# Optimization experiments

Measured on AMD Instinct MI355X. Metric: run time of the kernel, lower is better.

The kernel has to match this reference:

```python
import jax, jax.numpy as jnp
import numpy as np

D_MODEL = 1024
NUM_HEADS = 16
HEAD_DIM = D_MODEL // NUM_HEADS


def setup_inputs() -> dict:
    key = jax.random.key(0)
    kx, kq, kk, kv, ko = jax.random.split(key, 5)
    B, S = 4, 2048
    scale = 1.0 / np.sqrt(D_MODEL)
    return {
        "x": jax.random.normal(kx, (B, S, D_MODEL), dtype=jnp.float32),
        # bias-free linear weights, torch convention [out, in]
        "wq": jax.random.normal(kq, (D_MODEL, D_MODEL), dtype=jnp.float32) * scale,
        "wk": jax.random.normal(kk, (D_MODEL, D_MODEL), dtype=jnp.float32) * scale,
        "wv": jax.random.normal(kv, (D_MODEL, D_MODEL), dtype=jnp.float32) * scale,
        "wo": jax.random.normal(ko, (D_MODEL, D_MODEL), dtype=jnp.float32) * scale,
    }


def reference(x, wq, wk, wv, wo):
    B, S, D = x.shape
    H, Hd = NUM_HEADS, HEAD_DIM
    # projections (y = x @ W^T), reshape to [B, H, S, Hd]
    def proj(w):
        return jnp.einsum('bsd,ed->bse', x, w).reshape(B, S, H, Hd).transpose(0, 2, 1, 3)
    q, k, v = proj(wq), proj(wk), proj(wv)
    # scaled dot-product attention with causal mask
    scores = jnp.einsum('bhqd,bhkd->bhqk', q, k) / jnp.sqrt(jnp.asarray(Hd, x.dtype))
    causal = jnp.tril(jnp.ones((S, S), dtype=bool))  # [S, S]
    scores = jnp.where(causal[None, None], scores, jnp.asarray(-jnp.inf, x.dtype))
    attn = jax.nn.softmax(scores, axis=-1)
    out = jnp.einsum('bhqk,bhkd->bhqd', attn, v)  # [B, H, S, Hd]
    out = out.transpose(0, 2, 1, 3).reshape(B, S, D)
    return jnp.einsum('bsd,ed->bse', out, wo)
```

## Files before the change

kernel.cpp:

```cpp
#include <hip/hip_runtime.h>
#include <hip/hip_bf16.h>
#include <math.h>


#define S_LEN 2048
#define DM    1024
#define NH    16
#define HD    64
#define M_ROWS 8192

typedef __attribute__((ext_vector_type(8))) short bf16x8;
typedef __attribute__((ext_vector_type(4))) float f32x4;
typedef __attribute__((ext_vector_type(16))) float f32x16;

__device__ __forceinline__ float bf2f(unsigned short u) {
  union { unsigned int i; float f; } c; c.i = ((unsigned int)u) << 16; return c.f;
}
__device__ __forceinline__ unsigned short f2bf(float f) {
  unsigned int x = __float_as_uint(f);
  if ((x & 0x7fffffffu) > 0x7f800000u) return (unsigned short)0x7fc0u;
  return (unsigned short)((x + 0x7fffu + ((x >> 16) & 1u)) >> 16);
}
__device__ __forceinline__ void gl_lds16(const unsigned short* g, unsigned short* l) {
  __builtin_amdgcn_global_load_lds(
      (const __attribute__((address_space(1))) unsigned int*)g,
      (__attribute__((address_space(3))) unsigned int*)l, 16, 0, 0);
}

#define FENCE() asm volatile("" ::: "memory")

__global__ __launch_bounds__(256) void cvt_bf16(const float* __restrict__ in,
                                                unsigned short* __restrict__ out) {
  const int i = blockIdx.x * 256 + threadIdx.x;
  float4 a = ((const float4*)in)[2 * i];
  float4 b = ((const float4*)in)[2 * i + 1];
  ushort4 r0, r1;
  r0.x = f2bf(a.x); r0.y = f2bf(a.y); r0.z = f2bf(a.z); r0.w = f2bf(a.w);
  r1.x = f2bf(b.x); r1.y = f2bf(b.y); r1.z = f2bf(b.z); r1.w = f2bf(b.w);
  ((ushort4*)out)[2 * i] = r0;
  ((ushort4*)out)[2 * i + 1] = r1;
}

__global__ __launch_bounds__(256) void cvt_w3(const float* __restrict__ w0,
                                              const float* __restrict__ w1,
                                              const float* __restrict__ w2,
                                              unsigned short* __restrict__ out) {
  const int idx = blockIdx.x;
  const int which = idx >> 9;
  const float* src = (which == 0) ? w0 : (which == 1) ? w1 : w2;
  unsigned short* dst = out + (size_t)which * (DM * DM);
  const int i = (idx & 511) * 256 + threadIdx.x;
  float4 a = ((const float4*)src)[2 * i];
  float4 b = ((const float4*)src)[2 * i + 1];
  ushort4 r0, r1;
  r0.x = f2bf(a.x); r0.y = f2bf(a.y); r0.z = f2bf(a.z); r0.w = f2bf(a.w);
  r1.x = f2bf(b.x); r1.y = f2bf(b.y); r1.z = f2bf(b.z); r1.w = f2bf(b.w);
  ((ushort4*)dst)[2 * i] = r0;
  ((ushort4*)dst)[2 * i + 1] = r1;
}

template <int OUT_MODE>
__global__ __launch_bounds__(256, 2) void gemm_bt(const unsigned short* __restrict__ A,
                                                  const unsigned short* __restrict__ Wall,
                                                  unsigned short* __restrict__ outB,
                                                  float* __restrict__ outF) {
  __shared__ __align__(16) unsigned short As[3 * 4096];
  __shared__ __align__(16) unsigned short Bs[3 * 4096];
  const int m0 = blockIdx.x * 128;
  const int n0 = blockIdx.y * 128;
  const int tid = threadIdx.x;
  const int lane = tid & 63, w = tid >> 6;
  const int quad = lane >> 4, l15 = lane & 15;
  const int wr = w >> 1, wc = w & 1;

  const unsigned short* agA = A    + (size_t)(m0 + lane) * DM + w * 8;
  const unsigned short* bgB = Wall + (size_t)(n0 + lane) * DM + w * 8;
  const int lA0 = w * 1024;
  const int lB0 = w * 1024;
  const int raA = quad * 1024 + (wr * 64 + l15) * 8;
  const int raB = quad * 1024 + (wc * 64 + l15) * 8;

  f32x4 acc[4][4];
#pragma unroll
  for (int i = 0; i < 4; ++i)
#pragma unroll
    for (int j = 0; j < 4; ++j) { acc[i][j].x = 0.f; acc[i][j].y = 0.f; acc[i][j].z = 0.f; acc[i][j].w = 0.f; }

#define STAGE4(T, SB) do {                                                   \
    const unsigned short* ap_ = agA + (size_t)(T) * 32;                      \
    const unsigned short* bp_ = bgB + (size_t)(T) * 32;                      \
    gl_lds16(ap_,           &As[(SB) * 4096 + lA0]);                         \
    gl_lds16(ap_ + 64 * DM, &As[(SB) * 4096 + lA0 + 512]);                   \
    gl_lds16(bp_,           &Bs[(SB) * 4096 + lB0]);                         \
    gl_lds16(bp_ + 64 * DM, &Bs[(SB) * 4096 + lB0 + 512]);                   \
  } while (0)

#define COMPUTE(CB) do {                                                     \
    bf16x8 af_[4], bq_[4];                                                   \
    _Pragma("unroll")                                                        \
    for (int mi = 0; mi < 4; ++mi)                                           \
      af_[mi] = *(const bf16x8*)&As[(CB) * 4096 + raA + mi * 128];           \
    _Pragma("unroll")                                                        \
    for (int ni = 0; ni < 4; ++ni)                                           \
      bq_[ni] = *(const bf16x8*)&Bs[(CB) * 4096 + raB + ni * 128];           \
    __builtin_amdgcn_s_setprio(1);                                           \
    _Pragma("unroll")                                                        \
    for (int mi = 0; mi < 4; ++mi)                                           \
      _Pragma("unroll")                                                      \
      for (int ni = 0; ni < 4; ++ni)                                         \
        acc[mi][ni] = __builtin_amdgcn_mfma_f32_16x16x32_bf16(af_[mi], bq_[ni], acc[mi][ni], 0, 0, 0); \
    __builtin_amdgcn_s_setprio(0);                                           \
  } while (0)

#define SUBSTEP(T, SB, CB) do {                                              \
    asm volatile("s_waitcnt vmcnt(4)" ::: "memory");                         \
    __builtin_amdgcn_s_barrier();                                            \
    FENCE();                                                                 \
    STAGE4((T), (SB));                                                       \
    COMPUTE(CB);                                                             \
    FENCE();                                                                 \
  } while (0)

  STAGE4(0, 0);
  STAGE4(1, 1);

  for (int t = 0; t < 30; t += 3) {
    SUBSTEP(t + 2, 2, 0);
    SUBSTEP(t + 3, 0, 1);
    SUBSTEP(t + 4, 1, 2);
  }
  asm volatile("s_waitcnt vmcnt(4)" ::: "memory");
  __builtin_amdgcn_s_barrier();
  FENCE();
  COMPUTE(0);
  asm volatile("s_waitcnt vmcnt(0)" ::: "memory");
  __builtin_amdgcn_s_barrier();
  FENCE();
  COMPUTE(1);

#undef SUBSTEP
#undef COMPUTE
#undef STAGE4

  const float oscale = (OUT_MODE == 0 && n0 < 1024) ? 0.125f : 1.0f;
#pragma unroll
  for (int mi = 0; mi < 4; ++mi) {
#pragma unroll
    for (int reg = 0; reg < 4; ++reg) {
      const int m = m0 + wr * 64 + mi * 16 + quad * 4 + reg;
#pragma unroll
      for (int ni = 0; ni < 4; ++ni) {
        const int e = n0 + wc * 64 + ni * 16 + l15;
        const float v = acc[mi][ni][reg];
        if (OUT_MODE == 0) {
          const int z = e >> 10;
          const int e10 = e & 1023;
          const int b = m >> 11, s = m & (S_LEN - 1);
          const int h = e10 >> 6, hd = e10 & 63;
          outB[(size_t)z * (M_ROWS * DM) +
               (((size_t)(b * NH + h)) * S_LEN + s) * HD + hd] = f2bf(v * oscale);
        } else {
          outF[(size_t)m * DM + e] = v;
        }
      }
    }
  }
}

__global__ __launch_bounds__(256, 4) void attn_mfma(const unsigned short* __restrict__ Q,
                                                    const unsigned short* __restrict__ K,
                                                    const unsigned short* __restrict__ V,
                                                    unsigned short* __restrict__ O) {
  __shared__ unsigned short Ks[64][72];
  __shared__ unsigned short Vt[64][72];
  const int bh = blockIdx.x;
  const int bx = 15 - (int)blockIdx.y;
  const int tid = threadIdx.x;
  const int w = tid >> 6, lane = tid & 63;
  const int l31 = lane & 31, hi = lane >> 5;
  const size_t base = (size_t)bh * S_LEN * HD;
  const int b = bh >> 4, h = bh & 15;
  const int wq0 = bx * 128 + w * 32;
  const int diag_jt = 2 * bx + (w >> 1);
  const int jt_blk = 2 * bx + 1;
  const int kr0 = tid >> 3, kc0 = (tid & 7) * 8;
  const int vs = (tid & 31) * 2, vh = (tid >> 5) * 8;

  bf16x8 qb[4];
#pragma unroll
  for (int ds = 0; ds < 4; ++ds)
    qb[ds] = *(const bf16x8*)(Q + base + (size_t)(wq0 + l31) * HD + ds * 16 + hi * 8);

  f32x16 o0, o1;
#pragma unroll
  for (int r = 0; r < 16; ++r) { o0[r] = 0.f; o1[r] = 0.f; }
  float l_acc = 0.f;

  for (int jt = 0; jt <= jt_blk; ++jt) {
    __syncthreads();
    {
      const unsigned short* kgp = K + base + (size_t)jt * 64 * HD;
      const unsigned short* vgp = V + base + (size_t)jt * 64 * HD;
      *(uint4*)&Ks[kr0][kc0]      = *(const uint4*)(kgp + kr0 * HD + kc0);
      *(uint4*)&Ks[kr0 + 32][kc0] = *(const uint4*)(kgp + (kr0 + 32) * HD + kc0);
      uint4 r0 = *(const uint4*)(vgp + (size_t)vs * HD + vh);
      uint4 r1 = *(const uint4*)(vgp + (size_t)(vs + 1) * HD + vh);
      const unsigned int* a0 = (const unsigned int*)&r0;
      const unsigned int* a1 = (const unsigned int*)&r1;
#pragma unroll
      for (int j = 0; j < 4; ++j) {
        *(unsigned int*)&Vt[vh + 2 * j][vs]     = __builtin_amdgcn_perm(a1[j], a0[j], 0x05040100u);
        *(unsigned int*)&Vt[vh + 2 * j + 1][vs] = __builtin_amdgcn_perm(a1[j], a0[j], 0x07060302u);
      }
    }
    __syncthreads();

    if (jt <= diag_jt) {
      const bool diag = (jt == diag_jt);
      for (int kb = 0; kb < 2; ++kb) {
        const bool kb_zero = diag && ((w & 1) == 0) && (kb == 1);
        const bool kb_part = diag && (kb == (w & 1));
        if (kb_zero) continue;

        f32x16 sa;
#pragma unroll
        for (int r = 0; r < 16; ++r) sa[r] = 0.f;
        __builtin_amdgcn_s_setprio(1);
#pragma unroll
        for (int ds = 0; ds < 4; ++ds) {
          bf16x8 kf = *(const bf16x8*)&Ks[kb * 32 + l31][ds * 16 + hi * 8];
          sa = __builtin_amdgcn_mfma_f32_32x32x16_bf16(kf, qb[ds], sa, 0, 0, 0);
        }
        __builtin_amdgcn_s_setprio(0);

        float p[16];
        if (kb_part) {
#pragma unroll
          for (int r = 0; r < 16; ++r) {
            const int krel = (r & 3) + 8 * (r >> 2) + 4 * hi;
            p[r] = __expf((l31 >= krel) ? sa[r] : -1.0e30f);
          }
        } else {
#pragma unroll
          for (int r = 0; r < 16; ++r) p[r] = __expf(sa[r]);
        }
        l_acc += (((p[0] + p[1]) + (p[2] + p[3])) + ((p[4] + p[5]) + (p[6] + p[7])))
               + (((p[8] + p[9]) + (p[10] + p[11])) + ((p[12] + p[13]) + (p[14] + p[15])));

        unsigned int pk[8], sk[8];
#pragma unroll
        for (int g = 0; g < 4; ++g) {
          pk[2 * g]     = __builtin_amdgcn_perm(__float_as_uint(p[4 * g + 1]), __float_as_uint(p[4 * g]),     0x07060302u);
          pk[2 * g + 1] = __builtin_amdgcn_perm(__float_as_uint(p[4 * g + 3]), __float_as_uint(p[4 * g + 2]), 0x07060302u);
        }
#pragma unroll
        for (int i = 0; i < 8; ++i) sk[i] = (unsigned int)__shfl_xor((int)pk[i], 32);

#pragma unroll
        for (int sl = 0; sl < 2; ++sl) {
          const int g0 = 2 * sl, g1 = 2 * sl + 1;
          union { unsigned int u[4]; bf16x8 v; } fa;
          fa.u[0] = hi ? sk[2 * g1]     : pk[2 * g0];
          fa.u[1] = hi ? sk[2 * g1 + 1] : pk[2 * g0 + 1];
          fa.u[2] = hi ? pk[2 * g1]     : sk[2 * g0];
          fa.u[3] = hi ? pk[2 * g1 + 1] : sk[2 * g0 + 1];
          const int s = kb * 2 + sl;
          bf16x8 v0 = *(const bf16x8*)&Vt[l31][s * 16 + hi * 8];
          bf16x8 v1 = *(const bf16x8*)&Vt[32 + l31][s * 16 + hi * 8];
          __builtin_amdgcn_s_setprio(1);
          o0 = __builtin_amdgcn_mfma_f32_32x32x16_bf16(fa.v, v0, o0, 0, 0, 0);
          o1 = __builtin_amdgcn_mfma_f32_32x32x16_bf16(fa.v, v1, o1, 0, 0, 0);
          __builtin_amdgcn_s_setprio(0);
        }
      }
    }
  }

  const float lf = l_acc + __shfl_xor(l_acc, 32);
  const float inv = 1.0f / lf;
#pragma unroll
  for (int r = 0; r < 16; ++r) {
    const int qrel = (r & 3) + 8 * (r >> 2) + 4 * hi;
    const float invr = __shfl(inv, qrel);
    const size_t orow = (size_t)(b * S_LEN + wq0 + qrel) * DM + h * HD;
    O[orow + l31]      = f2bf(o0[r] * invr);
    O[orow + 32 + l31] = f2bf(o1[r] * invr);
  }
}

extern "C" void kernel_launch(void* const* d_in, const int* in_sizes, int n_in,
                              void* d_out, int out_size, void* d_ws, size_t ws_size,
                              hipStream_t stream) {
  const float* x  = (const float*)d_in[0];
  const float* wq = (const float*)d_in[1];
  const float* wk = (const float*)d_in[2];
  const float* wv = (const float*)d_in[3];
  const float* wo = (const float*)d_in[4];

  unsigned short* Qb = (unsigned short*)d_ws;
  unsigned short* Kb = Qb + (size_t)M_ROWS * DM;
  unsigned short* Vb = Kb + (size_t)M_ROWS * DM;
  unsigned short* Xb = Vb + (size_t)M_ROWS * DM;
  unsigned short* Ob = Xb;
  (void)Kb; (void)Vb;

  unsigned short* Wstash = (unsigned short*)d_out;

  dim3 bb(256);

  hipLaunchKernelGGL(cvt_bf16, dim3((M_ROWS * DM) / 2048), bb, 0, stream, x, Xb);
  hipLaunchKernelGGL(cvt_w3, dim3(3 * (DM * DM) / 2048), bb, 0, stream, wq, wk, wv, Wstash);
  hipLaunchKernelGGL((gemm_bt<0>), dim3(M_ROWS / 128, 3 * DM / 128), bb, 0, stream,
                     Xb, Wstash, Qb, (float*)nullptr);
  hipLaunchKernelGGL(attn_mfma, dim3(64, 16), bb, 0, stream, Qb, Qb + (size_t)M_ROWS * DM,
                     Qb + 2 * (size_t)M_ROWS * DM, Ob);
  hipLaunchKernelGGL(cvt_bf16, dim3((DM * DM) / 2048), bb, 0, stream, wo, Qb);
  hipLaunchKernelGGL((gemm_bt<1>), dim3(M_ROWS / 128, DM / 128), bb, 0, stream,
                     Ob, Qb, (unsigned short*)nullptr, (float*)d_out);
}
```

Before: 212.4 us.

## Widen GEMM tiles to 128x256 with 8 waves and K=64 ping-phase pipeline

The projection GEMMs now use 512-thread blocks computing 128x256 output tiles, with a K step of 64 per stage and a triple-buffered LDS ring. Each iteration is split into four phases, and global-to-LDS staging for the next tile is interleaved between MFMA groups. This is meant to raise arithmetic intensity and reuse of A, and to overlap loads with compute. In exchange, LDS use grows to about 144KB per block, which likely limits occupancy to one block per CU, barriers per K step increase, and the grid shrinks.

Result: slower. 236.9 us (+11.5%).

```diff
diff --git a/kernel.cpp b/kernel.cpp
--- a/kernel.cpp
+++ b/kernel.cpp
@@ -60,25 +60,25 @@
 }
 
 template <int OUT_MODE>
-__global__ __launch_bounds__(256, 2) void gemm_bt(const unsigned short* __restrict__ A,
+__global__ __launch_bounds__(512, 2) void gemm_bt(const unsigned short* __restrict__ A,
                                                   const unsigned short* __restrict__ Wall,
                                                   unsigned short* __restrict__ outB,
                                                   float* __restrict__ outF) {
-  __shared__ __align__(16) unsigned short As[3 * 4096];
-  __shared__ __align__(16) unsigned short Bs[3 * 4096];
+  __shared__ __align__(16) unsigned short As[3 * 8192];
+  __shared__ __align__(16) unsigned short Bs[3 * 16384];
   const int m0 = blockIdx.x * 128;
-  const int n0 = blockIdx.y * 128;
+  const int n0 = blockIdx.y * 256;
   const int tid = threadIdx.x;
   const int lane = tid & 63, w = tid >> 6;
   const int quad = lane >> 4, l15 = lane & 15;
-  const int wr = w >> 1, wc = w & 1;
+  const int wr = w >> 2, wc = w & 3;
 
   const unsigned short* agA = A    + (size_t)(m0 + lane) * DM + w * 8;
   const unsigned short* bgB = Wall + (size_t)(n0 + lane) * DM + w * 8;
-  const int lA0 = w * 1024;
-  const int lB0 = w * 1024;
-  const int raA = quad * 1024 + (wr * 64 + l15) * 8;
-  const int raB = quad * 1024 + (wc * 64 + l15) * 8;
+  const int sA0 = w * 1024;
+  const int sB0 = w * 2048;
+  const int aRd = quad * 1024 + (wr * 64 + l15) * 8;
+  const int bRd = quad * 2048 + (wc * 64 + l15) * 8;
 
   f32x4 acc[4][4];
 #pragma unroll
@@ -86,61 +86,85 @@
 #pragma unroll
     for (int j = 0; j < 4; ++j) { acc[i][j].x = 0.f; acc[i][j].y = 0.f; acc[i][j].z = 0.f; acc[i][j].w = 0.f; }
 
-#define STAGE4(T, SB) do {                                                   \
-    const unsigned short* ap_ = agA + (size_t)(T) * 32;                      \
-    const unsigned short* bp_ = bgB + (size_t)(T) * 32;                      \
-    gl_lds16(ap_,           &As[(SB) * 4096 + lA0]);                         \
-    gl_lds16(ap_ + 64 * DM, &As[(SB) * 4096 + lA0 + 512]);                   \
-    gl_lds16(bp_,           &Bs[(SB) * 4096 + lB0]);                         \
-    gl_lds16(bp_ + 64 * DM, &Bs[(SB) * 4096 + lB0 + 512]);                   \
-  } while (0)
-
-#define COMPUTE(CB) do {                                                     \
-    bf16x8 af_[4], bq_[4];                                                   \
-    _Pragma("unroll")                                                        \
-    for (int mi = 0; mi < 4; ++mi)                                           \
-      af_[mi] = *(const bf16x8*)&As[(CB) * 4096 + raA + mi * 128];           \
-    _Pragma("unroll")                                                        \
-    for (int ni = 0; ni < 4; ++ni)                                           \
-      bq_[ni] = *(const bf16x8*)&Bs[(CB) * 4096 + raB + ni * 128];           \
+#define MFMA_(a_, b_, c_) __builtin_amdgcn_mfma_f32_16x16x32_bf16((a_), (b_), (c_), 0, 0, 0)
+#define LD_A(C_, MI_, KS_) (*(const bf16x8*)&As[(C_) * 8192 + (KS_) * 4096 + aRd + (MI_) * 128])
+#define LD_B(C_, NI_, KS_) (*(const bf16x8*)&Bs[(C_) * 16384 + (KS_) * 8192 + bRd + (NI_) * 128])
+
+#define STG_A(T_, S_) do {                                                   \
+    const unsigned short* p_ = agA + (size_t)(T_) * 64;                      \
+    gl_lds16(p_,           &As[(S_) * 8192 + sA0]);                          \
+    gl_lds16(p_ + 64 * DM, &As[(S_) * 8192 + sA0 + 512]);                    \
+  } while (0)
+#define STG_B01(T_, S_) do {                                                 \
+    const unsigned short* p_ = bgB + (size_t)(T_) * 64;                      \
+    gl_lds16(p_,           &Bs[(S_) * 16384 + sB0]);                         \
+    gl_lds16(p_ + 64 * DM, &Bs[(S_) * 16384 + sB0 + 512]);                   \
+  } while (0)
+#define STG_B23(T_, S_) do {                                                 \
+    const unsigned short* p_ = bgB + (size_t)(T_) * 64 + 128 * DM;           \
+    gl_lds16(p_,           &Bs[(S_) * 16384 + sB0 + 1024]);                  \
+    gl_lds16(p_ + 64 * DM, &Bs[(S_) * 16384 + sB0 + 1536]);                  \
+  } while (0)
+
+#define VM6  asm volatile("s_waitcnt vmcnt(6)" ::: "memory")
+#define VM0  asm volatile("s_waitcnt vmcnt(0)" ::: "memory")
+
+#define PHASE(C_, MI0_, NI0_, STAGE_STMT_, WAIT_STMT_) do {                  \
+    bf16x8 a00 = LD_A(C_, MI0_,     0), a01 = LD_A(C_, MI0_,     1);         \
+    bf16x8 a10 = LD_A(C_, MI0_ + 1, 0), a11 = LD_A(C_, MI0_ + 1, 1);         \
+    bf16x8 b00 = LD_B(C_, NI0_,     0), b01 = LD_B(C_, NI0_,     1);         \
+    bf16x8 b10 = LD_B(C_, NI0_ + 1, 0), b11 = LD_B(C_, NI0_ + 1, 1);         \
+    STAGE_STMT_;                                                             \
+    WAIT_STMT_;                                                              \
+    FENCE();                                                                 \
+    __builtin_amdgcn_s_barrier();                                            \
+    asm volatile("s_waitcnt lgkmcnt(0)" ::: "memory");                       \
     __builtin_amdgcn_s_setprio(1);                                           \
-    _Pragma("unroll")                                                        \
-    for (int mi = 0; mi < 4; ++mi)                                           \
-      _Pragma("unroll")                                                      \
-      for (int ni = 0; ni < 4; ++ni)                                         \
-        acc[mi][ni] = __builtin_amdgcn_mfma_f32_16x16x32_bf16(af_[mi], bq_[ni], acc[mi][ni], 0, 0, 0); \
+    acc[MI0_    ][NI0_    ] = MFMA_(a00, b00, acc[MI0_    ][NI0_    ]);      \
+    acc[MI0_    ][NI0_ + 1] = MFMA_(a00, b10, acc[MI0_    ][NI0_ + 1]);      \
+    acc[MI0_ + 1][NI0_    ] = MFMA_(a10, b00, acc[MI0_ + 1][NI0_    ]);      \
+    acc[MI0_ + 1][NI0_ + 1] = MFMA_(a10, b10, acc[MI0_ + 1][NI0_ + 1]);      \
+    acc[MI0_    ][NI0_    ] = MFMA_(a01, b01, acc[MI0_    ][NI0_    ]);      \
+    acc[MI0_    ][NI0_ + 1] = MFMA_(a01, b11, acc[MI0_    ][NI0_ + 1]);      \
+    acc[MI0_ + 1][NI0_    ] = MFMA_(a11, b01, acc[MI0_ + 1][NI0_    ]);      \
+    acc[MI0_ + 1][NI0_ + 1] = MFMA_(a11, b11, acc[MI0_ + 1][NI0_ + 1]);      \
     __builtin_amdgcn_s_setprio(0);                                           \
-  } while (0)
-
-#define SUBSTEP(T, SB, CB) do {                                              \
-    asm volatile("s_waitcnt vmcnt(4)" ::: "memory");                         \
+    FENCE();                                                                 \
     __builtin_amdgcn_s_barrier();                                            \
-    FENCE();                                                                 \
-    STAGE4((T), (SB));                                                       \
-    COMPUTE(CB);                                                             \
-    FENCE();                                                                 \
-  } while (0)
-
-  STAGE4(0, 0);
-  STAGE4(1, 1);
-
-  for (int t = 0; t < 30; t += 3) {
-    SUBSTEP(t + 2, 2, 0);
-    SUBSTEP(t + 3, 0, 1);
-    SUBSTEP(t + 4, 1, 2);
+  } while (0)
+
+#define ITER(T_, C_, S_, STG_, ENDW_) do {                                   \
+    PHASE(C_, 0, 0, if (STG_) STG_A((T_) + 2, S_), (void)0);                 \
+    PHASE(C_, 0, 2, if (STG_) STG_B01((T_) + 2, S_), (void)0);               \
+    PHASE(C_, 2, 0, if (STG_) STG_B23((T_) + 2, S_), (void)0);               \
+    PHASE(C_, 2, 2, (void)0, ENDW_);                                         \
+  } while (0)
+
+  STG_A(0, 0); STG_B01(0, 0); STG_B23(0, 0);
+  STG_A(1, 1); STG_B01(1, 1); STG_B23(1, 1);
+  VM6;
+  __builtin_amdgcn_s_barrier();
+
+  for (int t = 0; t < 12; t += 3) {
+    ITER(t,     0, 2, true, VM6);
+    ITER(t + 1, 1, 0, true, VM6);
+    ITER(t + 2, 2, 1, true, VM6);
   }
-  asm volatile("s_waitcnt vmcnt(4)" ::: "memory");
-  __builtin_amdgcn_s_barrier();
-  FENCE();
-  COMPUTE(0);
-  asm volatile("s_waitcnt vmcnt(0)" ::: "memory");
-  __builtin_amdgcn_s_barrier();
-  FENCE();
-  COMPUTE(1);
-
-#undef SUBSTEP
-#undef COMPUTE
-#undef STAGE4
+  ITER(12, 0, 2, true, VM6);
+  ITER(13, 1, 0, true, VM6);
+  ITER(14, 2, 0, false, VM0);
+  ITER(15, 0, 0, false, (void)0);
+
+#undef ITER
+#undef PHASE
+#undef VM0
+#undef VM6
+#undef STG_B23
+#undef STG_B01
+#undef STG_A
+#undef LD_B
+#undef LD_A
+#undef MFMA_
 
   const float oscale = (OUT_MODE == 0 && n0 < 1024) ? 0.125f : 1.0f;
 #pragma unroll
@@ -307,14 +331,15 @@
   unsigned short* Wstash = (unsigned short*)d_out;
 
   dim3 bb(256);
+  dim3 gb(512);
 
   hipLaunchKernelGGL(cvt_bf16, dim3((M_ROWS * DM) / 2048), bb, 0, stream, x, Xb);
   hipLaunchKernelGGL(cvt_w3, dim3(3 * (DM * DM) / 2048), bb, 0, stream, wq, wk, wv, Wstash);
-  hipLaunchKernelGGL((gemm_bt<0>), dim3(M_ROWS / 128, 3 * DM / 128), bb, 0, stream,
+  hipLaunchKernelGGL((gemm_bt<0>), dim3(M_ROWS / 128, 3 * DM / 256), gb, 0, stream,
                      Xb, Wstash, Qb, (float*)nullptr);
   hipLaunchKernelGGL(attn_mfma, dim3(64, 16), bb, 0, stream, Qb, Qb + (size_t)M_ROWS * DM,
                      Qb + 2 * (size_t)M_ROWS * DM, Ob);
   hipLaunchKernelGGL(cvt_bf16, dim3((DM * DM) / 2048), bb, 0, stream, wo, Qb);
-  hipLaunchKernelGGL((gemm_bt<1>), dim3(M_ROWS / 128, DM / 128), bb, 0, stream,
+  hipLaunchKernelGGL((gemm_bt<1>), dim3(M_ROWS / 128, DM / 256), gb, 0, stream,
                      Ob, Qb, (unsigned short*)nullptr, (float*)d_out);
 }
```
